# Performance work log

Hardware: AMD Instinct MI355X
Metric: run time of the kernel (lower is better)

## Reference

```python
import jax, jax.numpy as jnp
import numpy as np

HIDDEN = 2048
NUM_Q_HEADS = 16
NUM_KV_HEADS = 4
HEAD_DIM = HIDDEN // NUM_Q_HEADS  # 128
KV_REP = NUM_Q_HEADS // NUM_KV_HEADS  # 4
KV_DIM = HEAD_DIM * NUM_KV_HEADS


def setup_inputs() -> dict:
    key = jax.random.key(0)
    ks = jax.random.split(key, 9)
    B, S = 2, 2048
    s_in = 1.0 / np.sqrt(HIDDEN)
    return {
        "hidden_states": jax.random.normal(ks[0], (B, S, HIDDEN), dtype=jnp.float32),
        "Wq": jax.random.normal(ks[1], (HIDDEN, HIDDEN), dtype=jnp.float32) * s_in,
        "bq": jnp.zeros((HIDDEN,), dtype=jnp.float32),
        "Wk": jax.random.normal(ks[2], (HIDDEN, KV_DIM), dtype=jnp.float32) * s_in,
        "bk": jnp.zeros((KV_DIM,), dtype=jnp.float32),
        "Wv": jax.random.normal(ks[3], (HIDDEN, KV_DIM), dtype=jnp.float32) * s_in,
        "bv": jnp.zeros((KV_DIM,), dtype=jnp.float32),
        "Wo": jax.random.normal(ks[4], (HIDDEN, HIDDEN), dtype=jnp.float32) * s_in,
        "bo": jnp.zeros((HIDDEN,), dtype=jnp.float32),
    }


def reference(hidden_states, Wq, bq, Wk, bk, Wv, bv, Wo, bo):
    B, S, H = hidden_states.shape
    # projections
    q = hidden_states @ Wq + bq  # [B,S,H]
    k = hidden_states @ Wk + bk  # [B,S,KV_DIM]
    v = hidden_states @ Wv + bv  # [B,S,KV_DIM]
    # [B, heads, S, head_dim]
    q = q.reshape(B, S, NUM_Q_HEADS, HEAD_DIM).transpose(0, 2, 1, 3)
    k = k.reshape(B, S, NUM_KV_HEADS, HEAD_DIM).transpose(0, 2, 1, 3)
    v = v.reshape(B, S, NUM_KV_HEADS, HEAD_DIM).transpose(0, 2, 1, 3)
    # repeat_interleave KV heads to match q heads
    k = jnp.repeat(k, KV_REP, axis=1)  # [B,Hq,S,hd]
    v = jnp.repeat(v, KV_REP, axis=1)
    scale = 1.0 / np.sqrt(HEAD_DIM)
    scores = jnp.einsum('bhqd,bhkd->bhqk', q, k) * scale  # [B,Hq,S,S]
    causal = jnp.triu(jnp.ones((S, S), dtype=bool), k=1)
    scores = jnp.where(causal[None, None], -jnp.inf, scores)
    probs = jax.nn.softmax(scores, axis=-1)
    ctx = jnp.einsum('bhqk,bhkd->bhqd', probs, v)  # [B,Hq,S,hd]
    ctx = ctx.transpose(0, 2, 1, 3).reshape(B, S, H)
    return ctx @ Wo + bo
```

## Files before the change

### kernel.cpp

```cpp
#include <hip/hip_runtime.h>
#include <hip/hip_bf16.h>
#include <stdint.h>

#define SEQ 2048
#define BATCH 2
#define NTOK (SEQ * BATCH)
#define HID 2048
#define NQH 16
#define NKVH 4
#define HD 128
#define KVD 512

typedef __bf16 bf16x8 __attribute__((ext_vector_type(8)));
typedef float f32x4 __attribute__((ext_vector_type(4)));
typedef float f32x16 __attribute__((ext_vector_type(16)));
typedef unsigned int u32;

__device__ __forceinline__ unsigned short f2bf(float f) {
    uint32_t u = __builtin_bit_cast(uint32_t, f);
    uint32_t r = (u + 0x7fffu + ((u >> 16) & 1u)) >> 16;
    return (unsigned short)r;
}

__device__ __forceinline__ u32 cvtpk(float lo, float hi) {
    u32 r;
    asm("v_cvt_pk_bf16_f32 %0, %1, %2" : "=v"(r) : "v"(lo), "v"(hi));
    return r;
}

__device__ __forceinline__ void gload16(const void* g, void* l) {
    __builtin_amdgcn_global_load_lds((const __attribute__((address_space(1))) u32*)g,
                                     (__attribute__((address_space(3))) u32*)l, 16, 0, 0);
}

#define BARRIER()  asm volatile("s_barrier" ::: "memory")
#define LGKM0()    do { asm volatile("s_waitcnt lgkmcnt(0)" ::: "memory"); \
                        __builtin_amdgcn_sched_barrier(0); } while (0)
#define VMCNT(n)   asm volatile("s_waitcnt vmcnt(" #n ")" ::: "memory")

__global__ void cvt_f32_bf16(const float* __restrict__ in, unsigned short* __restrict__ out, int n4) {
    int i = blockIdx.x * blockDim.x + threadIdx.x;
    int stride = gridDim.x * blockDim.x;
    for (; i < n4; i += stride) {
        float4 v = ((const float4*)in)[i];
        ushort4 o;
        o.x = f2bf(v.x); o.y = f2bf(v.y); o.z = f2bf(v.z); o.w = f2bf(v.w);
        ((ushort4*)out)[i] = o;
    }
}

__global__ __launch_bounds__(256) void transpose_all(const float* __restrict__ Wq,
                                                     const float* __restrict__ Wk,
                                                     const float* __restrict__ Wv,
                                                     const float* __restrict__ Wo,
                                                     unsigned short* __restrict__ Wqkvt,
                                                     unsigned short* __restrict__ Wot) {
    __shared__ unsigned short tile[64][72];
    const int y = blockIdx.y;
    const float* W;
    unsigned short* dst;
    int N, ny;
    if (y < 32)      { W = Wq; dst = Wqkvt;                        N = 2048; ny = y; }
    else if (y < 40) { W = Wk; dst = Wqkvt + (size_t)2048 * HID;   N = 512;  ny = y - 32; }
    else if (y < 48) { W = Wv; dst = Wqkvt + (size_t)2560 * HID;   N = 512;  ny = y - 40; }
    else             { W = Wo; dst = Wot;                          N = 2048; ny = y - 48; }
    const int k0 = blockIdx.x * 64, n0 = ny * 64;
    const int t = threadIdx.x;
    const int r = t >> 4;
    const int c4 = (t & 15) * 4;
    #pragma unroll
    for (int i = 0; i < 4; i++) {
        int row = r + i * 16;
        float4 v = *(const float4*)&W[(size_t)(k0 + row) * N + n0 + c4];
        tile[row][c4 + 0] = f2bf(v.x);
        tile[row][c4 + 1] = f2bf(v.y);
        tile[row][c4 + 2] = f2bf(v.z);
        tile[row][c4 + 3] = f2bf(v.w);
    }
    __syncthreads();
    #pragma unroll
    for (int i = 0; i < 4; i++) {
        int nrow = r + i * 16;
        ushort4 o;
        o.x = tile[c4 + 0][nrow];
        o.y = tile[c4 + 1][nrow];
        o.z = tile[c4 + 2][nrow];
        o.w = tile[c4 + 3][nrow];
        *(ushort4*)&dst[(size_t)(n0 + nrow) * HID + k0 + c4] = o;
    }
}

__global__ __launch_bounds__(512, 2) void gemm_qkv(const unsigned short* __restrict__ A,
                                                   const unsigned short* __restrict__ Bt,
                                                   const float* __restrict__ bq,
                                                   const float* __restrict__ bk,
                                                   const float* __restrict__ bv,
                                                   unsigned short* __restrict__ Qo,
                                                   unsigned short* __restrict__ Ko,
                                                   unsigned short* __restrict__ Vo) {
    __shared__ __align__(16) char LDSRAW[131072];
    const int NTT = HID / 64;
    const int bid = blockIdx.x;
    const int swz = (bid % 8) * 24 + bid / 8;
    const int m0 = (swz % 16) * 256;
    const int nb = swz / 16;
    const int n0 = nb * 256;
    const int tid = threadIdx.x;
    const int lane = tid & 63, w = tid >> 6;
    const int wm = w >> 2, wn = w & 3;
    const int l16 = lane & 15, lg = lane >> 4;

    f32x4 acc[2][4][4] = {};

    auto stageHalf = [&](int ts, int mtx, int kh) {
        if (ts >= NTT) return;
        const unsigned short* src = mtx ? (Bt + (size_t)n0 * HID) : (A + (size_t)m0 * HID);
        const int region = mtx * 65536 + (ts & 1) * 32768 + kh * 16384;
        #pragma unroll
        for (int j = 0; j < 2; j++) {
            int c = j * 512 + tid;
            int row = c >> 2, s = c & 3;
            int cg = s ^ ((row >> 1) & 3);
            gload16(&src[(size_t)row * HID + ts * 64 + kh * 32 + cg * 8],
                    LDSRAW + region + (j * 512 + w * 64) * 16);
        }
    };
    auto ldsA = [&](int buf, int kh, int mq, bf16x8 (&dst)[4]) {
        #pragma unroll
        for (int mf = 0; mf < 4; mf++) {
            int row = wm * 128 + mq * 64 + mf * 16 + l16;
            int slot = lg ^ ((row >> 1) & 3);
            dst[mf] = *(const bf16x8*)(LDSRAW + buf * 32768 + kh * 16384 + row * 64 + slot * 16);
        }
    };
    auto ldsB = [&](int buf, int kh, bf16x8 (&dst)[4]) {
        #pragma unroll
        for (int nf = 0; nf < 4; nf++) {
            int row = wn * 64 + nf * 16 + l16;
            int slot = lg ^ ((row >> 1) & 3);
            dst[nf] = *(const bf16x8*)(LDSRAW + 65536 + buf * 32768 + kh * 16384 + row * 64 + slot * 16);
        }
    };
    auto mfma16 = [&](f32x4 (&ac)[4][4], bf16x8 (&a4)[4], bf16x8 (&b4)[4]) {
        __builtin_amdgcn_s_setprio(1);
        #pragma unroll
        for (int mf = 0; mf < 4; mf++)
            #pragma unroll
            for (int nf = 0; nf < 4; nf++)
                ac[mf][nf] = __builtin_amdgcn_mfma_f32_16x16x32_bf16(a4[mf], b4[nf], ac[mf][nf], 0, 0, 0);
        __builtin_amdgcn_s_setprio(0);
    };

    stageHalf(0, 0, 0); stageHalf(0, 1, 0); stageHalf(0, 0, 1); stageHalf(0, 1, 1);
    stageHalf(1, 0, 0); stageHalf(1, 1, 0);
    VMCNT(4);
    BARRIER();

    for (int t = 0; t < NTT; t++) {
        const int buf = t & 1;
        bf16x8 a4[4], b4[4];
        ldsA(buf, 0, 0, a4); ldsB(buf, 0, b4);
        stageHalf(t + 1, 0, 1);
        BARRIER(); LGKM0();
        mfma16(acc[0], a4, b4);
        BARRIER();
        ldsA(buf, 0, 1, a4);
        stageHalf(t + 1, 1, 1);
        BARRIER(); LGKM0();
        mfma16(acc[1], a4, b4);
        BARRIER();
        ldsA(buf, 1, 0, a4); ldsB(buf, 1, b4);
        stageHalf(t + 2, 0, 0);
        if (t == NTT - 1) { VMCNT(0); }
        BARRIER(); LGKM0();
        mfma16(acc[0], a4, b4);
        BARRIER();
        ldsA(buf, 1, 1, a4);
        stageHalf(t + 2, 1, 0);
        if (t < NTT - 1) { VMCNT(4); }
        BARRIER(); LGKM0();
        mfma16(acc[1], a4, b4);
        BARRIER();
    }

    const float sc = 0.08838834764831845f;
    #pragma unroll
    for (int mq = 0; mq < 2; mq++) {
        #pragma unroll
        for (int mf = 0; mf < 4; mf++) {
            int row = m0 + wm * 128 + mq * 64 + mf * 16 + lg * 4;
            #pragma unroll
            for (int nf = 0; nf < 4; nf++) {
                int col = n0 + wn * 64 + nf * 16 + l16;
                #pragma unroll
                for (int r = 0; r < 4; r++) {
                    float v = acc[mq][mf][nf][r];
                    int rr = row + r;
                    if (nb < 8) {
                        v = (v + bq[col]) * sc;
                        Qo[(size_t)rr * HID + col] = f2bf(v);
                    } else if (nb < 10) {
                        int c = col - 2048;
                        v += bk[c];
                        Ko[(size_t)rr * KVD + c] = f2bf(v);
                    } else {
                        int c = col - 2560;
                        v += bv[c];
                        int b = rr >> 11, s = rr & (SEQ - 1);
                        Vo[((size_t)b * KVD + c) * SEQ + s] = f2bf(v);
                    }
                }
            }
        }
    }
}

__global__ __launch_bounds__(256) void gemm_o(const unsigned short* __restrict__ A,
                                              const unsigned short* __restrict__ Bt,
                                              const float* __restrict__ bias,
                                              float* __restrict__ out1) {
    __shared__ unsigned short Asm[2][128 * 64];
    __shared__ unsigned short Bsm[2][128 * 64];
    const int m0 = blockIdx.x * 128;
    const int n0 = blockIdx.y * 128;
    const int t = threadIdx.x;
    const int lane = t & 63, w = t >> 6;
    const int wr = (w >> 1) * 64, wc = (w & 1) * 64;
    const int l16 = lane & 15, lg = lane >> 4;

    f32x4 acc[4][4] = {};

    auto stage = [&](int buf, int kt) {
        const int k0 = kt * 64;
        #pragma unroll
        for (int it = 0; it < 4; it++) {
            int base = it * 256 + w * 64;
            int qc = base + lane;
            int row = qc >> 3, c = qc & 7;
            int col = ((c ^ (row & 7)) << 3);
            gload16(&A[(size_t)(m0 + row) * HID + k0 + col], (char*)&Asm[buf][0] + base * 16);
            gload16(&Bt[(size_t)(n0 + row) * HID + k0 + col], (char*)&Bsm[buf][0] + base * 16);
        }
    };

    stage(0, 0);
    __syncthreads();
    int buf = 0;
    for (int kt = 0; kt < HID / 64; kt++) {
        if (kt < HID / 64 - 1) stage(buf ^ 1, kt + 1);
        const char* Ab = (const char*)&Asm[buf][0];
        const char* Bb = (const char*)&Bsm[buf][0];
        #pragma unroll
        for (int kk = 0; kk < 2; kk++) {
            bf16x8 af[4], bfr[4];
            #pragma unroll
            for (int m = 0; m < 4; m++) {
                int row = wr + m * 16 + l16;
                af[m] = *(const bf16x8*)(Ab + row * 128 + (((kk * 4 + lg) ^ (row & 7)) << 4));
            }
            #pragma unroll
            for (int n = 0; n < 4; n++) {
                int row = wc + n * 16 + l16;
                bfr[n] = *(const bf16x8*)(Bb + row * 128 + (((kk * 4 + lg) ^ (row & 7)) << 4));
            }
            #pragma unroll
            for (int m = 0; m < 4; m++)
                #pragma unroll
                for (int n = 0; n < 4; n++)
                    acc[m][n] = __builtin_amdgcn_mfma_f32_16x16x32_bf16(af[m], bfr[n], acc[m][n], 0, 0, 0);
        }
        __syncthreads();
        buf ^= 1;
    }
    #pragma unroll
    for (int m = 0; m < 4; m++) {
        int row = m0 + wr + m * 16 + lg * 4;
        #pragma unroll
        for (int n = 0; n < 4; n++) {
            int col = n0 + wc + n * 16 + l16;
            #pragma unroll
            for (int r = 0; r < 4; r++)
                out1[(size_t)(row + r) * HID + col] = acc[m][n][r] + bias[col];
        }
    }
}

__global__ __launch_bounds__(256, 2) void attn(const unsigned short* __restrict__ Q,
                                               const unsigned short* __restrict__ K,
                                               const unsigned short* __restrict__ Vt,
                                               unsigned short* __restrict__ ctx) {
    __shared__ unsigned short Ksm[2][64 * 128];
    __shared__ unsigned short Vsm[2][128 * 64];
    const int n = blockIdx.x;
    const int qt = 15 - (n >> 5);
    const int bh = n & 31;
    const int b = bh >> 4, h = bh & 15, hk = h >> 2;
    const int t = threadIdx.x, w = t >> 6, lane = t & 63;
    const int lam = lane & 31, hi = lane >> 5;
    const int qw = qt * 128 + w * 32;
    const int qg = qw + lam;
    const size_t qrowbase = (size_t)b * SEQ + qw;

    const unsigned short* Kg = K + (size_t)b * SEQ * KVD + hk * HD;
    const unsigned short* Vg = Vt + ((size_t)b * KVD + hk * HD) * SEQ;

    bf16x8 qf[8];
    #pragma unroll
    for (int kc = 0; kc < 8; kc++)
        qf[kc] = *(const bf16x8*)&Q[(qrowbase + lam) * HID + h * HD + kc * 16 + hi * 8];

    f32x16 oacc[4] = {};
    float m = -1e30f, l = 0.f;

    auto stage = [&](int buf, int kt) {
        const int kvb = kt * 64;
        #pragma unroll
        for (int it = 0; it < 4; it++) {
            int base = it * 256 + w * 64;
            int qc = base + lane;
            {
                int row = qc >> 4, c = qc & 15;
                gload16(&Kg[(size_t)(kvb + row) * KVD + ((c ^ (row & 7)) << 3)],
                        (char*)&Ksm[buf][0] + base * 16);
            }
            {
                int row = qc >> 3, c = qc & 7;
                gload16(&Vg[(size_t)row * SEQ + kvb + ((c ^ (row & 7)) << 3)],
                        (char*)&Vsm[buf][0] + base * 16);
            }
        }
    };

    const int ntile = 2 * qt + 2;
    stage(0, 0);
    __syncthreads();
    int buf = 0;
    for (int kt = 0; kt < ntile; kt++) {
        const int kvb = kt * 64;
        if (kt + 1 < ntile) stage(buf ^ 1, kt + 1);
        if (kvb <= qw + 31) {
            const char* Kb = (const char*)&Ksm[buf][0];
            const char* Vb = (const char*)&Vsm[buf][0];
            f32x16 st0 = {}, st1 = {};
            #pragma unroll
            for (int kc = 0; kc < 8; kc++) {
                int coff = (kc * 32 + hi * 16) ^ ((lam & 7) << 4);
                bf16x8 kf0 = *(const bf16x8*)(Kb + lam * 256 + coff);
                bf16x8 kf1 = *(const bf16x8*)(Kb + (32 + lam) * 256 + coff);
                st0 = __builtin_amdgcn_mfma_f32_32x32x16_bf16(kf0, qf[kc], st0, 0, 0, 0);
                st1 = __builtin_amdgcn_mfma_f32_32x32x16_bf16(kf1, qf[kc], st1, 0, 0, 0);
            }
            if (kvb + 63 > qw) {
                #pragma unroll
                for (int r = 0; r < 16; r++) {
                    int krow = (r & 3) + 8 * (r >> 2) + 4 * hi;
                    if (kvb + krow > qg) st0[r] = -1e30f;
                    if (kvb + 32 + krow > qg) st1[r] = -1e30f;
                }
            }
            float tmax = st0[0];
            #pragma unroll
            for (int r = 1; r < 16; r++) tmax = fmaxf(tmax, st0[r]);
            #pragma unroll
            for (int r = 0; r < 16; r++) tmax = fmaxf(tmax, st1[r]);
            tmax = fmaxf(tmax, __shfl_xor(tmax, 32));
            float mn = fmaxf(m, tmax);
            float sf = __expf(m - mn);
            m = mn;
            float rs = 0.f;
            #pragma unroll
            for (int r = 0; r < 16; r++) { st0[r] = __expf(st0[r] - mn); rs += st0[r]; }
            #pragma unroll
            for (int r = 0; r < 16; r++) { st1[r] = __expf(st1[r] - mn); rs += st1[r]; }
            rs += __shfl_xor(rs, 32);
            l = l * sf + rs;
            #pragma unroll
            for (int dc = 0; dc < 4; dc++)
                #pragma unroll
                for (int r = 0; r < 16; r++) oacc[dc][r] *= sf;
            u32 pw0[4][2], pw1[4][2];
            #pragma unroll
            for (int g = 0; g < 4; g++) {
                pw0[g][0] = cvtpk(st0[4 * g], st0[4 * g + 1]);
                pw0[g][1] = cvtpk(st0[4 * g + 2], st0[4 * g + 3]);
                pw1[g][0] = cvtpk(st1[4 * g], st1[4 * g + 1]);
                pw1[g][1] = cvtpk(st1[4 * g + 2], st1[4 * g + 3]);
            }
            #pragma unroll
            for (int kc = 0; kc < 4; kc++) {
                const u32 (*pw)[2] = (kc >> 1) ? pw1 : pw0;
                int g0 = (kc & 1) * 2;
                u32 own0 = hi ? pw[g0 + 1][0] : pw[g0][0];
                u32 own1 = hi ? pw[g0 + 1][1] : pw[g0][1];
                u32 off0 = hi ? pw[g0][0] : pw[g0 + 1][0];
                u32 off1 = hi ? pw[g0][1] : pw[g0 + 1][1];
                u32 xw0 = __shfl_xor(off0, 32);
                u32 xw1 = __shfl_xor(off1, 32);
                int4 paw;
                paw.x = hi ? xw0 : own0;
                paw.y = hi ? xw1 : own1;
                paw.z = hi ? own0 : xw0;
                paw.w = hi ? own1 : xw1;
                bf16x8 pa = __builtin_bit_cast(bf16x8, paw);
                #pragma unroll
                for (int dc = 0; dc < 4; dc++) {
                    bf16x8 vf = *(const bf16x8*)(Vb + (dc * 32 + lam) * 128 +
                                                 ((kc * 32 + hi * 16) ^ ((lam & 7) << 4)));
                    oacc[dc] = __builtin_amdgcn_mfma_f32_32x32x16_bf16(vf, pa, oacc[dc], 0, 0, 0);
                }
            }
        }
        __syncthreads();
        buf ^= 1;
    }

    float inv = 1.f / l;
    char* osm = (char*)&Ksm[0][0] + w * 8192;
    #pragma unroll
    for (int dc = 0; dc < 4; dc++)
        #pragma unroll
        for (int r = 0; r < 16; r += 2) {
            int d = dc * 32 + (r & 3) + 8 * (r >> 2) + 4 * hi;
            u32 wd = cvtpk(oacc[dc][r] * inv, oacc[dc][r + 1] * inv);
            *(u32*)(osm + lam * 256 + ((d * 2) ^ ((lam & 7) << 4))) = wd;
        }
    __syncthreads();
    const int q2 = lane >> 1, half = lane & 1;
    #pragma unroll
    for (int cc = 0; cc < 8; cc++) {
        bf16x8 v = *(const bf16x8*)(osm + q2 * 256 + (((half * 8 + cc) * 16) ^ ((q2 & 7) << 4)));
        *(bf16x8*)&ctx[(qrowbase + q2) * HID + h * HD + half * 64 + cc * 8] = v;
    }
}

extern "C" void kernel_launch(void* const* d_in, const int* in_sizes, int n_in,
                              void* d_out, int out_size, void* d_ws, size_t ws_size,
                              hipStream_t stream) {
    const float* X  = (const float*)d_in[0];
    const float* Wq = (const float*)d_in[1];
    const float* bq = (const float*)d_in[2];
    const float* Wk = (const float*)d_in[3];
    const float* bk = (const float*)d_in[4];
    const float* Wv = (const float*)d_in[5];
    const float* bv = (const float*)d_in[6];
    const float* Wo = (const float*)d_in[7];
    const float* bo = (const float*)d_in[8];
    float* out = (float*)d_out;

    const size_t MB = 1u << 20;
    char* ws = (char*)d_ws;
    if (ws_size < 76 * MB) return;
    unsigned short* Xb    = (unsigned short*)(ws + 0 * MB);
    unsigned short* Wqkvt = (unsigned short*)(ws + 16 * MB);
    unsigned short* Wot   = (unsigned short*)(ws + 28 * MB);
    unsigned short* Qb    = (unsigned short*)(ws + 36 * MB);
    unsigned short* Kb    = (unsigned short*)(ws + 52 * MB);
    unsigned short* Vtb   = (unsigned short*)(ws + 56 * MB);
    unsigned short* Ctx   = (unsigned short*)(ws + 60 * MB);

    cvt_f32_bf16<<<2048, 256, 0, stream>>>(X, Xb, NTOK * HID / 4);
    transpose_all<<<dim3(32, 80), 256, 0, stream>>>(Wq, Wk, Wv, Wo, Wqkvt, Wot);

    gemm_qkv<<<dim3(192), 512, 0, stream>>>(Xb, Wqkvt, bq, bk, bv, Qb, Kb, Vtb);

    attn<<<dim3(512), 256, 0, stream>>>(Qb, Kb, Vtb, Ctx);

    gemm_o<<<dim3(32, 16), 256, 0, stream>>>(Ctx, Wot, bo, out);
}
```

Measured before the change: 222.0 us.

## Merge GEMM sub-phases, add lazy softmax rescale and MFMA priority hints

```diff
diff --git a/kernel.cpp b/kernel.cpp
--- a/kernel.cpp
+++ b/kernel.cpp
@@ -141,15 +141,6 @@
             dst[nf] = *(const bf16x8*)(LDSRAW + 65536 + buf * 32768 + kh * 16384 + row * 64 + slot * 16);
         }
     };
-    auto mfma16 = [&](f32x4 (&ac)[4][4], bf16x8 (&a4)[4], bf16x8 (&b4)[4]) {
-        __builtin_amdgcn_s_setprio(1);
-        #pragma unroll
-        for (int mf = 0; mf < 4; mf++)
-            #pragma unroll
-            for (int nf = 0; nf < 4; nf++)
-                ac[mf][nf] = __builtin_amdgcn_mfma_f32_16x16x32_bf16(a4[mf], b4[nf], ac[mf][nf], 0, 0, 0);
-        __builtin_amdgcn_s_setprio(0);
-    };
 
     stageHalf(0, 0, 0); stageHalf(0, 1, 0); stageHalf(0, 0, 1); stageHalf(0, 1, 1);
     stageHalf(1, 0, 0); stageHalf(1, 1, 0);
@@ -158,28 +149,41 @@
 
     for (int t = 0; t < NTT; t++) {
         const int buf = t & 1;
-        bf16x8 a4[4], b4[4];
-        ldsA(buf, 0, 0, a4); ldsB(buf, 0, b4);
+        bf16x8 aLo[4], aHi[4], b4[4];
+        ldsA(buf, 0, 0, aLo); ldsA(buf, 0, 1, aHi); ldsB(buf, 0, b4);
         stageHalf(t + 1, 0, 1);
-        BARRIER(); LGKM0();
-        mfma16(acc[0], a4, b4);
-        BARRIER();
-        ldsA(buf, 0, 1, a4);
         stageHalf(t + 1, 1, 1);
         BARRIER(); LGKM0();
-        mfma16(acc[1], a4, b4);
+        __builtin_amdgcn_s_setprio(1);
+        #pragma unroll
+        for (int mf = 0; mf < 4; mf++)
+            #pragma unroll
+            for (int nf = 0; nf < 4; nf++)
+                acc[0][mf][nf] = __builtin_amdgcn_mfma_f32_16x16x32_bf16(aLo[mf], b4[nf], acc[0][mf][nf], 0, 0, 0);
+        #pragma unroll
+        for (int mf = 0; mf < 4; mf++)
+            #pragma unroll
+            for (int nf = 0; nf < 4; nf++)
+                acc[1][mf][nf] = __builtin_amdgcn_mfma_f32_16x16x32_bf16(aHi[mf], b4[nf], acc[1][mf][nf], 0, 0, 0);
+        __builtin_amdgcn_s_setprio(0);
         BARRIER();
-        ldsA(buf, 1, 0, a4); ldsB(buf, 1, b4);
+        ldsA(buf, 1, 0, aLo); ldsA(buf, 1, 1, aHi); ldsB(buf, 1, b4);
         stageHalf(t + 2, 0, 0);
-        if (t == NTT - 1) { VMCNT(0); }
+        stageHalf(t + 2, 1, 0);
+        if (t == NTT - 1) { VMCNT(0); } else { VMCNT(4); }
         BARRIER(); LGKM0();
-        mfma16(acc[0], a4, b4);
-        BARRIER();
-        ldsA(buf, 1, 1, a4);
-        stageHalf(t + 2, 1, 0);
-        if (t < NTT - 1) { VMCNT(4); }
-        BARRIER(); LGKM0();
-        mfma16(acc[1], a4, b4);
+        __builtin_amdgcn_s_setprio(1);
+        #pragma unroll
+        for (int mf = 0; mf < 4; mf++)
+            #pragma unroll
+            for (int nf = 0; nf < 4; nf++)
+                acc[0][mf][nf] = __builtin_amdgcn_mfma_f32_16x16x32_bf16(aLo[mf], b4[nf], acc[0][mf][nf], 0, 0, 0);
+        #pragma unroll
+        for (int mf = 0; mf < 4; mf++)
+            #pragma unroll
+            for (int nf = 0; nf < 4; nf++)
+                acc[1][mf][nf] = __builtin_amdgcn_mfma_f32_16x16x32_bf16(aHi[mf], b4[nf], acc[1][mf][nf], 0, 0, 0);
+        __builtin_amdgcn_s_setprio(0);
         BARRIER();
     }
 
@@ -342,6 +346,7 @@
             const char* Kb = (const char*)&Ksm[buf][0];
             const char* Vb = (const char*)&Vsm[buf][0];
             f32x16 st0 = {}, st1 = {};
+            __builtin_amdgcn_s_setprio(1);
             #pragma unroll
             for (int kc = 0; kc < 8; kc++) {
                 int coff = (kc * 32 + hi * 16) ^ ((lam & 7) << 4);
@@ -350,6 +355,7 @@
                 st0 = __builtin_amdgcn_mfma_f32_32x32x16_bf16(kf0, qf[kc], st0, 0, 0, 0);
                 st1 = __builtin_amdgcn_mfma_f32_32x32x16_bf16(kf1, qf[kc], st1, 0, 0, 0);
             }
+            __builtin_amdgcn_s_setprio(0);
             if (kvb + 63 > qw) {
                 #pragma unroll
                 for (int r = 0; r < 16; r++) {
@@ -364,20 +370,23 @@
             #pragma unroll
             for (int r = 0; r < 16; r++) tmax = fmaxf(tmax, st1[r]);
             tmax = fmaxf(tmax, __shfl_xor(tmax, 32));
-            float mn = fmaxf(m, tmax);
-            float sf = __expf(m - mn);
-            m = mn;
+            if (!__all(tmax - m <= 8.0f)) {
+                float mn = fmaxf(m, tmax);
+                float sf = __expf(m - mn);
+                m = mn;
+                l *= sf;
+                #pragma unroll
+                for (int dc = 0; dc < 4; dc++)
+                    #pragma unroll
+                    for (int r = 0; r < 16; r++) oacc[dc][r] *= sf;
+            }
             float rs = 0.f;
             #pragma unroll
-            for (int r = 0; r < 16; r++) { st0[r] = __expf(st0[r] - mn); rs += st0[r]; }
-            #pragma unroll
-            for (int r = 0; r < 16; r++) { st1[r] = __expf(st1[r] - mn); rs += st1[r]; }
+            for (int r = 0; r < 16; r++) { st0[r] = __expf(st0[r] - m); rs += st0[r]; }
+            #pragma unroll
+            for (int r = 0; r < 16; r++) { st1[r] = __expf(st1[r] - m); rs += st1[r]; }
             rs += __shfl_xor(rs, 32);
-            l = l * sf + rs;
-            #pragma unroll
-            for (int dc = 0; dc < 4; dc++)
-                #pragma unroll
-                for (int r = 0; r < 16; r++) oacc[dc][r] *= sf;
+            l += rs;
             u32 pw0[4][2], pw1[4][2];
             #pragma unroll
             for (int g = 0; g < 4; g++) {
@@ -402,12 +411,14 @@
                 paw.z = hi ? own0 : xw0;
                 paw.w = hi ? own1 : xw1;
                 bf16x8 pa = __builtin_bit_cast(bf16x8, paw);
+                __builtin_amdgcn_s_setprio(1);
                 #pragma unroll
                 for (int dc = 0; dc < 4; dc++) {
                     bf16x8 vf = *(const bf16x8*)(Vb + (dc * 32 + lam) * 128 +
                                                  ((kc * 32 + hi * 16) ^ ((lam & 7) << 4)));
                     oacc[dc] = __builtin_amdgcn_mfma_f32_32x32x16_bf16(vf, pa, oacc[dc], 0, 0, 0);
                 }
+                __builtin_amdgcn_s_setprio(0);
             }
         }
         __syncthreads();
```

New measurement: 230.4 us. 1.04x slower.
